# Kernel optimization log

Measured on AMD Instinct MI355X. Metric: run time of the kernel, lower is better.

The kernel has to match this reference:

```python
import jax, jax.numpy as jnp
import numpy as np

B, L, E, H = 4, 1024, 2048, 16
DH = E // H
SCALE_BASE = 512.0


def _rotate_every_two(x):
    x1 = x[..., ::2]
    x2 = x[..., 1::2]
    return jnp.stack([-x2, x1], axis=-1).reshape(x.shape)


def _xpos(x, downscale):
    # x: [BH, L, Dh]; non-incremental path => offset = 0
    length = x.shape[1]
    head_dim = x.shape[-1]
    min_pos = -(length // 2)
    positions = jnp.arange(min_pos, length + min_pos, dtype=jnp.float32)  # [L]
    base = (jnp.arange(0, head_dim, 2, dtype=jnp.float32) + 0.4 * head_dim) / (1.4 * head_dim)  # [Dh/2]
    scale = base[None, :] ** (positions[:, None] / SCALE_BASE)  # [L, Dh/2]
    # fixed_pos_embedding over `scale` (seq_len=L, dim=Dh/2), positions 0..L-1
    dim = head_dim // 2
    inv_freq = 1.0 / (10000.0 ** (jnp.arange(0, dim, dtype=jnp.float32) / dim))
    sinusoid = jnp.arange(length, dtype=jnp.float32)[:, None] * inv_freq[None, :]
    sin, cos = jnp.sin(sinusoid), jnp.cos(sinusoid)
    if downscale:
        scale = 1.0 / scale
    sin_s = jnp.repeat(sin * scale, 2, axis=-1)  # duplicate_interleave -> [L, Dh]
    cos_s = jnp.repeat(cos * scale, 2, axis=-1)
    return x * cos_s + _rotate_every_two(x) * sin_s


def setup_inputs() -> dict:
    key = jax.random.key(0)
    ks = jax.random.split(key, 6)
    w_std = 1.0 / np.sqrt(E)
    query = jax.random.normal(ks[0], (B, L, E), dtype=jnp.float32)
    Wq = jax.random.normal(ks[1], (E, E), dtype=jnp.float32) * w_std
    Wk = jax.random.normal(ks[2], (E, E), dtype=jnp.float32) * w_std
    Wv = jax.random.normal(ks[3], (E, E), dtype=jnp.float32) * w_std
    Wo = jax.random.normal(ks[4], (E, E), dtype=jnp.float32) * w_std
    bq = jnp.zeros((E,), jnp.float32)
    bk = jnp.zeros((E,), jnp.float32)
    bv = jnp.zeros((E,), jnp.float32)
    bo = jnp.zeros((E,), jnp.float32)
    # causal additive mask [L, L]: 0 on/below diag, large negative above
    attn_mask = jnp.where(jnp.triu(jnp.ones((L, L), bool), k=1), -1e9, 0.0).astype(jnp.float32)
    rel_pos = jax.random.normal(ks[5], (B * H, L, L), dtype=jnp.float32) * 0.02
    return {"query": query, "Wq": Wq, "bq": bq, "Wk": Wk, "bk": bk, "Wv": Wv,
            "bv": bv, "Wo": Wo, "bo": bo, "attn_mask": attn_mask, "rel_pos": rel_pos}


def reference(query, Wq, bq, Wk, bk, Wv, bv, Wo, bo, attn_mask, rel_pos):
    scaling = DH ** -0.5
    q = (query @ Wq.T + bq) * scaling
    k = query @ Wk.T + bk
    v = query @ Wv.T + bv

    def split(t):  # [B, L, E] -> [B*H, L, Dh]
        return t.reshape(B, L, H, DH).transpose(0, 2, 1, 3).reshape(B * H, L, DH)

    q, k, v = split(q), split(k), split(v)
    k = _xpos(k, downscale=True)
    q = _xpos(q, downscale=False)

    w = jnp.einsum('btd,bsd->bts', q, k)          # [B*H, L, L]
    w = jnp.nan_to_num(w) + attn_mask[None]
    w = w + rel_pos
    w = jax.nn.softmax(w.astype(jnp.float32), axis=-1).astype(w.dtype)
    attn = jnp.einsum('bts,bsd->btd', w, v)       # [B*H, L, Dh]
    attn = attn.reshape(B, H, L, DH).transpose(0, 2, 1, 3).reshape(B, L, E)
    out = attn @ Wo.T + bo
    attn_weights = w.reshape(B, H, L, L).transpose(1, 0, 2, 3)  # [H, B, L, L]
    return out, attn_weights
```

## Files before the change

### kernel.cpp

```cpp
#include <hip/hip_runtime.h>
#include <math.h>

#define BB 4
#define LL 1024
#define EE 2048
#define HH 16
#define DHD 128
#define NTOK 4096
#define NBH 64
#define OUT0_ELEMS 8388608

typedef __attribute__((ext_vector_type(8))) short short8;
typedef __attribute__((ext_vector_type(4))) float f32x4;
typedef __attribute__((ext_vector_type(4))) unsigned short ushort4v;
typedef __attribute__((ext_vector_type(8))) unsigned short ushort8v;

__device__ __forceinline__ unsigned short f2bf(float x) {
    union { float f; unsigned int u; } v; v.f = x;
    unsigned int r = v.u + 0x7FFFu + ((v.u >> 16) & 1u);
    return (unsigned short)(r >> 16);
}
__device__ __forceinline__ float bf2f(unsigned short h) {
    union { unsigned int u; float f; } v; v.u = ((unsigned int)h) << 16;
    return v.f;
}

__device__ __forceinline__ void gload16(const void* g, void* l) {
    __builtin_amdgcn_global_load_lds((const __attribute__((address_space(1))) void*)g,
                                     (__attribute__((address_space(3))) void*)l,
                                     16, 0, 0);
}

__global__ __launch_bounds__(256)
void cvt_all_k(const float* __restrict__ X, const float* __restrict__ Wq,
               const float* __restrict__ Wk, const float* __restrict__ Wv,
               const float* __restrict__ Wo, unsigned short* __restrict__ Xbf,
               unsigned short* __restrict__ Wqkvb, unsigned short* __restrict__ Wob) {
    size_t g = (size_t)(blockIdx.x * 256 + threadIdx.x) * 8;
    if (g >= 25165824u) return;
    const float* src;
    unsigned short* dst;
    if (g < 8388608u) {
        src = X + g; dst = Xbf + g;
    } else {
        size_t rr = g - 8388608u;
        int wi = (int)(rr >> 22);
        size_t o = rr & 4194303u;
        src = (wi == 0 ? Wq : wi == 1 ? Wk : wi == 2 ? Wv : Wo) + o;
        dst = (wi < 3 ? Wqkvb + ((size_t)wi << 22) : Wob) + o;
    }
    float4 a = *(const float4*)(src);
    float4 b = *(const float4*)(src + 4);
    ushort4v u, w;
    u.x = f2bf(a.x); u.y = f2bf(a.y); u.z = f2bf(a.z); u.w = f2bf(a.w);
    w.x = f2bf(b.x); w.y = f2bf(b.y); w.z = f2bf(b.z); w.w = f2bf(b.w);
    *(ushort4v*)(dst) = u;
    *(ushort4v*)(dst + 4) = w;
}

__global__ __launch_bounds__(64) void xpos_table_k(float4* __restrict__ tab) {
    int t = blockIdx.x;
    int j = threadIdx.x;
    float pos = (float)(t - 512);
    float base = (2.0f * (float)j + 51.2f) * (1.0f / 179.2f);
    float sc = powf(base, pos * (1.0f / 512.0f));
    float inv_freq = powf(10000.0f, -(float)j * (1.0f / 64.0f));
    float ang = (float)t * inv_freq;
    float s = sinf(ang);
    float c = cosf(ang);
    tab[(t << 6) | j] = make_float4(c * sc, s * sc, c / sc, s / sc);
}

__global__ __launch_bounds__(256)
void mmqkv_k(const unsigned short* __restrict__ Abf, const unsigned short* __restrict__ Wqkv,
             const float* __restrict__ bq, const float* __restrict__ bk,
             const float* __restrict__ bv, unsigned short* __restrict__ qb,
             unsigned short* __restrict__ kb, unsigned short* __restrict__ vt,
             const float4* __restrict__ tab, float scaling) {
    __shared__ alignas(16) unsigned short lA[128 * 32];
    __shared__ alignas(16) unsigned short lB[128 * 32];

    const int tid = threadIdx.x;
    const int lane = tid & 63;
    const int wave = tid >> 6;
    const int wr = wave >> 1, wc = wave & 1;
    const int fr = lane & 15, fq = lane >> 4;
    const int m0 = blockIdx.y * 128, n0 = blockIdx.x * 128;
    const int w = n0 >> 11;
    const float* bsel = (w == 0) ? bq : (w == 1) ? bk : bv;
    const float alpha = (w == 0) ? scaling : 1.0f;

    f32x4 acc[4][4];
#pragma unroll
    for (int i = 0; i < 4; ++i)
#pragma unroll
        for (int j = 0; j < 4; ++j) acc[i][j] = (f32x4){0.f, 0.f, 0.f, 0.f};

    for (int k0 = 0; k0 < 2048; k0 += 32) {
#pragma unroll
        for (int i = 0; i < 2; ++i) {
            int c = i * 256 + tid;
            int r = c >> 2, kc = c & 3;
            gload16(Abf + (size_t)(m0 + r) * 2048 + k0 + kc * 8, &lA[c * 8]);
        }
#pragma unroll
        for (int i = 0; i < 2; ++i) {
            int c = i * 256 + tid;
            int r = c >> 2, kc = c & 3;
            gload16(Wqkv + (size_t)(n0 + r) * 2048 + k0 + kc * 8, &lB[c * 8]);
        }
        __syncthreads();

        short8 afr[4], bfr[4];
#pragma unroll
        for (int mi = 0; mi < 4; ++mi)
            afr[mi] = *(const short8*)&lA[(wr * 64 + mi * 16 + fr) * 32 + fq * 8];
#pragma unroll
        for (int ni = 0; ni < 4; ++ni)
            bfr[ni] = *(const short8*)&lB[(wc * 64 + ni * 16 + fr) * 32 + fq * 8];
#pragma unroll
        for (int mi = 0; mi < 4; ++mi)
#pragma unroll
            for (int ni = 0; ni < 4; ++ni)
                acc[mi][ni] = __builtin_amdgcn_mfma_f32_16x16x32_bf16(
                    afr[mi], bfr[ni], acc[mi][ni], 0, 0, 0);
        __syncthreads();
    }

#pragma unroll
    for (int mi = 0; mi < 4; ++mi) {
#pragma unroll
        for (int ni = 0; ni < 4; ++ni) {
            int n = n0 + wc * 64 + ni * 16 + fr;
            int nn = n & 2047;
            int h = nn >> 7, d = nn & 127;
            float bias = bsel[nn];
#pragma unroll
            for (int r = 0; r < 4; ++r) {
                int m = m0 + wr * 64 + mi * 16 + fq * 4 + r;
                int b_ = m >> 10, t = m & 1023;
                float v = alpha * (acc[mi][ni][r] + bias);
                if (w < 2) {
                    float pv = __shfl_xor(v, 1);
                    float4 tb = tab[(t << 6) | (d >> 1)];
                    float c = (w == 0) ? tb.x : tb.z;
                    float s = (w == 0) ? tb.y : tb.w;
                    float rot = (d & 1) ? (v * c + pv * s) : (v * c - pv * s);
                    unsigned short* dst = (w == 0) ? qb : kb;
                    dst[(((size_t)(b_ * HH + h) << 10 | t) << 7) | d] = f2bf(rot);
                } else {
                    vt[((size_t)((b_ * HH + h) * 128 + d) << 10) | t] = f2bf(v);
                }
            }
        }
    }
}

__global__ __launch_bounds__(256)
void mmo_k(const unsigned short* __restrict__ Abf, const unsigned short* __restrict__ Bp,
           const float* __restrict__ bias, float* __restrict__ C) {
    __shared__ alignas(16) unsigned short lA[128 * 32];
    __shared__ alignas(16) unsigned short lB[128 * 32];

    const int tid = threadIdx.x;
    const int lane = tid & 63;
    const int wave = tid >> 6;
    const int wr = wave >> 1, wc = wave & 1;
    const int fr = lane & 15, fq = lane >> 4;
    const int m0 = blockIdx.y * 128, n0 = blockIdx.x * 128;

    f32x4 acc[4][4];
#pragma unroll
    for (int i = 0; i < 4; ++i)
#pragma unroll
        for (int j = 0; j < 4; ++j) acc[i][j] = (f32x4){0.f, 0.f, 0.f, 0.f};

    for (int k0 = 0; k0 < 2048; k0 += 32) {
#pragma unroll
        for (int i = 0; i < 2; ++i) {
            int c = i * 256 + tid;
            int r = c >> 2, kc = c & 3;
            gload16(Abf + (size_t)(m0 + r) * 2048 + k0 + kc * 8, &lA[c * 8]);
        }
#pragma unroll
        for (int i = 0; i < 2; ++i) {
            int c = i * 256 + tid;
            int r = c >> 2, kc = c & 3;
            gload16(Bp + (size_t)(n0 + r) * 2048 + k0 + kc * 8, &lB[c * 8]);
        }
        __syncthreads();

        short8 afr[4], bfr[4];
#pragma unroll
        for (int mi = 0; mi < 4; ++mi)
            afr[mi] = *(const short8*)&lA[(wr * 64 + mi * 16 + fr) * 32 + fq * 8];
#pragma unroll
        for (int ni = 0; ni < 4; ++ni)
            bfr[ni] = *(const short8*)&lB[(wc * 64 + ni * 16 + fr) * 32 + fq * 8];
#pragma unroll
        for (int mi = 0; mi < 4; ++mi)
#pragma unroll
            for (int ni = 0; ni < 4; ++ni)
                acc[mi][ni] = __builtin_amdgcn_mfma_f32_16x16x32_bf16(
                    afr[mi], bfr[ni], acc[mi][ni], 0, 0, 0);
        __syncthreads();
    }

#pragma unroll
    for (int mi = 0; mi < 4; ++mi)
#pragma unroll
        for (int ni = 0; ni < 4; ++ni)
#pragma unroll
            for (int r = 0; r < 4; ++r) {
                int m = m0 + wr * 64 + mi * 16 + fq * 4 + r;
                int n = n0 + wc * 64 + ni * 16 + fr;
                C[(size_t)m * EE + n] = acc[mi][ni][r] + bias[n];
            }
}

__global__ __launch_bounds__(256)
void scores_k(const unsigned short* __restrict__ qb, const unsigned short* __restrict__ kb,
              const float* __restrict__ rel, unsigned short* __restrict__ ebuf,
              float* __restrict__ psum) {
    __shared__ alignas(16) char smem[16384];
    unsigned short* lA = (unsigned short*)smem;
    unsigned short* lB = (unsigned short*)(smem + 8192);
    float* slab = (float*)smem;

    const int tid = threadIdx.x;
    const int lane = tid & 63, wave = tid >> 6;
    const int wr = wave >> 1, wc = wave & 1;
    const int fr = lane & 15, fq = lane >> 4;

    int idx = blockIdx.x;
    int tt = (int)((sqrtf(8.f * (float)idx + 1.f) - 1.f) * 0.5f);
    while ((tt + 1) * (tt + 2) / 2 <= idx) ++tt;
    while (tt * (tt + 1) / 2 > idx) --tt;
    const int ss = idx - tt * (tt + 1) / 2;
    const int t0 = tt << 7, s0 = ss << 7;
    const int bh = blockIdx.y;

    const unsigned short* Q = qb + ((size_t)bh << 17);
    const unsigned short* K = kb + ((size_t)bh << 17);

    f32x4 acc[4][4];
#pragma unroll
    for (int i = 0; i < 4; ++i)
#pragma unroll
        for (int j = 0; j < 4; ++j) acc[i][j] = (f32x4){0.f, 0.f, 0.f, 0.f};

    for (int k0 = 0; k0 < 128; k0 += 32) {
#pragma unroll
        for (int i = 0; i < 2; ++i) {
            int c = i * 256 + tid;
            int r = c >> 2, kc = c & 3;
            gload16(Q + (size_t)(t0 + r) * 128 + k0 + kc * 8, &lA[c * 8]);
        }
#pragma unroll
        for (int i = 0; i < 2; ++i) {
            int c = i * 256 + tid;
            int r = c >> 2, kc = c & 3;
            gload16(K + (size_t)(s0 + r) * 128 + k0 + kc * 8, &lB[c * 8]);
        }
        __syncthreads();

        short8 afr[4], bfr[4];
#pragma unroll
        for (int mi = 0; mi < 4; ++mi)
            afr[mi] = *(const short8*)&lA[(wr * 64 + mi * 16 + fr) * 32 + fq * 8];
#pragma unroll
        for (int ni = 0; ni < 4; ++ni)
            bfr[ni] = *(const short8*)&lB[(wc * 64 + ni * 16 + fr) * 32 + fq * 8];
#pragma unroll
        for (int mi = 0; mi < 4; ++mi)
#pragma unroll
            for (int ni = 0; ni < 4; ++ni)
                acc[mi][ni] = __builtin_amdgcn_mfma_f32_16x16x32_bf16(
                    afr[mi], bfr[ni], acc[mi][ni], 0, 0, 0);
        __syncthreads();
    }

    unsigned short* EO = ebuf + ((size_t)bh << 20);
    const float* RLb = rel + ((size_t)bh << 20);
#pragma unroll
    for (int sl = 0; sl < 4; ++sl) {
        if (wr == (sl >> 1)) {
#pragma unroll
            for (int mi2 = 0; mi2 < 2; ++mi2) {
                int mi = ((sl & 1) << 1) + mi2;
#pragma unroll
                for (int ni = 0; ni < 4; ++ni)
#pragma unroll
                    for (int r = 0; r < 4; ++r) {
                        int srow = (mi2 << 4) + (fq << 2) + r;
                        int col = (wc << 6) + (ni << 4) + fr;
                        slab[srow * 128 + (col ^ (((srow >> 2) & 3) << 4))] = acc[mi][ni][r];
                    }
            }
        }
        __syncthreads();
        {
            int srow = tid >> 3;
            int tg = t0 + (sl << 5) + srow;
            const float* RL = RLb + ((size_t)tg << 10) + s0;
            unsigned short* ER = EO + ((size_t)tg << 10) + s0;
            float rsum = 0.f;
#pragma unroll
            for (int c = 0; c < 4; ++c) {
                int col = ((tid & 7) << 2) + (c << 5);
                float4 sv = *(const float4*)&slab[srow * 128 + (col ^ (((srow >> 2) & 3) << 4))];
                float4 rl = *(const float4*)(RL + col);
                float4 e;
                e.x = (s0 + col     <= tg) ? __expf(sv.x + rl.x - 15.f) : 0.f;
                e.y = (s0 + col + 1 <= tg) ? __expf(sv.y + rl.y - 15.f) : 0.f;
                e.z = (s0 + col + 2 <= tg) ? __expf(sv.z + rl.z - 15.f) : 0.f;
                e.w = (s0 + col + 3 <= tg) ? __expf(sv.w + rl.w - 15.f) : 0.f;
                ushort4v h;
                h.x = f2bf(e.x); h.y = f2bf(e.y); h.z = f2bf(e.z); h.w = f2bf(e.w);
                *(ushort4v*)(ER + col) = h;
                rsum += e.x + e.y + e.z + e.w;
            }
            rsum += __shfl_xor(rsum, 1);
            rsum += __shfl_xor(rsum, 2);
            rsum += __shfl_xor(rsum, 4);
            if ((tid & 7) == 0)
                psum[((((size_t)bh << 10) + tg) << 3) + ss] = rsum;
        }
        __syncthreads();
    }
}

__global__ __launch_bounds__(256)
void pvw_k(const unsigned short* __restrict__ ebuf, const unsigned short* __restrict__ vt,
           const float* __restrict__ psum, float* __restrict__ attnP,
           unsigned short* __restrict__ am) {
    __shared__ alignas(16) unsigned short lE[64 * 64];
    __shared__ alignas(16) unsigned short lV[128 * 64];
    __shared__ float lInvF[64];

    const int tid = threadIdx.x;
    const int lane = tid & 63, wave = tid >> 6;
    const int wr = wave >> 1, wc = wave & 1;
    const int fr = lane & 15, fq = lane >> 4;
    const int strip = 15 - blockIdx.y;
    const int t0 = strip << 6;
    const int bh = blockIdx.x;
    const int hh = bh & 15, bb = bh >> 4;
    const int n_s = (t0 >> 6) + 1;

    const unsigned short* EB = ebuf + ((size_t)bh << 20) + ((size_t)t0 << 10);
    const unsigned short* Vb = vt + ((size_t)bh << 17);
    float* PO = attnP + (((size_t)(hh * BB + bb)) << 20) + ((size_t)t0 << 10);

    if (tid < 64) {
        const float* p = psum + ((((size_t)bh << 10) + t0 + tid) << 3);
        const int tt = t0 >> 7;
        float s = 0.f;
#pragma unroll
        for (int j = 0; j < 8; ++j) s += (j <= tt) ? p[j] : 0.f;
        lInvF[tid] = 1.f / s;
    }
    __syncthreads();

    f32x4 acc[2][4];
#pragma unroll
    for (int i = 0; i < 2; ++i)
#pragma unroll
        for (int j = 0; j < 4; ++j) acc[i][j] = (f32x4){0.f, 0.f, 0.f, 0.f};

    for (int j = 0; j < n_s; ++j) {
        int s0 = j << 6;
#pragma unroll
        for (int i = 0; i < 2; ++i) {
            int o = (i * 256 + tid) * 16;
            int r = o >> 7;
            int cb = (o & 127) ^ ((r & 7) << 4);
            gload16(EB + (size_t)r * 1024 + s0 + (cb >> 1), (char*)lE + o);
        }
#pragma unroll
        for (int i = 0; i < 4; ++i) {
            int o = (i * 256 + tid) * 16;
            int r = o >> 7;
            int cb = (o & 127) ^ ((r & 7) << 4);
            gload16(Vb + (size_t)r * 1024 + s0 + (cb >> 1), (char*)lV + o);
        }
        __syncthreads();

        {
            int row = tid >> 2, col0 = (tid & 3) << 4;
            float inv = lInvF[row];
            float* PR = PO + (size_t)row * 1024 + s0 + col0;
#pragma unroll
            for (int cc = 0; cc < 2; ++cc) {
                int cbyte = ((col0 + cc * 8) * 2) ^ ((row & 7) << 4);
                ushort8v ev = *(const ushort8v*)((const char*)lE + row * 128 + cbyte);
                float4 p0, p1;
                p0.x = bf2f(ev[0]) * inv; p0.y = bf2f(ev[1]) * inv;
                p0.z = bf2f(ev[2]) * inv; p0.w = bf2f(ev[3]) * inv;
                p1.x = bf2f(ev[4]) * inv; p1.y = bf2f(ev[5]) * inv;
                p1.z = bf2f(ev[6]) * inv; p1.w = bf2f(ev[7]) * inv;
                *(float4*)(PR + cc * 8) = p0;
                *(float4*)(PR + cc * 8 + 4) = p1;
            }
        }

#pragma unroll
        for (int ks = 0; ks < 2; ++ks) {
            short8 pf[2], vf[4];
#pragma unroll
            for (int mi = 0; mi < 2; ++mi) {
                int row = wr * 32 + mi * 16 + fr;
                int cb = (ks * 64 + fq * 16) ^ ((row & 7) << 4);
                pf[mi] = *(const short8*)((const char*)lE + row * 128 + cb);
            }
#pragma unroll
            for (int ni = 0; ni < 4; ++ni) {
                int row = wc * 64 + ni * 16 + fr;
                int cb = (ks * 64 + fq * 16) ^ ((row & 7) << 4);
                vf[ni] = *(const short8*)((const char*)lV + row * 128 + cb);
            }
#pragma unroll
            for (int mi = 0; mi < 2; ++mi)
#pragma unroll
                for (int ni = 0; ni < 4; ++ni)
                    acc[mi][ni] = __builtin_amdgcn_mfma_f32_16x16x32_bf16(
                        pf[mi], vf[ni], acc[mi][ni], 0, 0, 0);
        }
        __syncthreads();
    }

    {
        int row = tid >> 2;
        float4 z = make_float4(0.f, 0.f, 0.f, 0.f);
        for (int c = (n_s << 6) + ((tid & 3) << 2); c < 1024; c += 16)
            *(float4*)(PO + (size_t)row * 1024 + c) = z;
    }

#pragma unroll
    for (int mi = 0; mi < 2; ++mi)
#pragma unroll
        for (int ni = 0; ni < 4; ++ni)
#pragma unroll
            for (int r = 0; r < 4; ++r) {
                int tl = wr * 32 + mi * 16 + fq * 4 + r;
                int d = wc * 64 + ni * 16 + fr;
                float o = acc[mi][ni][r] * lInvF[tl];
                am[(((size_t)(bb * 1024 + t0 + tl)) << 11) + hh * 128 + d] = f2bf(o);
            }
}

extern "C" void kernel_launch(void* const* d_in, const int* in_sizes, int n_in,
                              void* d_out, int out_size, void* d_ws, size_t ws_size,
                              hipStream_t stream) {
    const float* query = (const float*)d_in[0];
    const float* Wq    = (const float*)d_in[1];
    const float* bq    = (const float*)d_in[2];
    const float* Wk    = (const float*)d_in[3];
    const float* bk    = (const float*)d_in[4];
    const float* Wv    = (const float*)d_in[5];
    const float* bv    = (const float*)d_in[6];
    const float* Wo    = (const float*)d_in[7];
    const float* bo    = (const float*)d_in[8];
    const float* rel   = (const float*)d_in[10];

    float* out    = (float*)d_out;
    float* attn_w = out + OUT0_ELEMS;

    char* w = (char*)d_ws;
    unsigned short* Xbf   = (unsigned short*)(w);
    unsigned short* Wqkvb = (unsigned short*)(w + (16 << 20));
    unsigned short* Wob   = (unsigned short*)(w + (40 << 20));
    unsigned short* qb    = (unsigned short*)(w + (48 << 20));
    unsigned short* kb    = (unsigned short*)(w + (64 << 20));
    unsigned short* vt    = (unsigned short*)(w + (80 << 20));
    unsigned short* am    = (unsigned short*)(w + (96 << 20));
    float4* tab           = (float4*)(w + (112 << 20));
    float* psum           = (float*)(w + (113u << 20));
    unsigned short* ebuf  = (unsigned short*)(w + (128u << 20));

    const float scaling = 0.08838834764831845f;

    xpos_table_k<<<LL, 64, 0, stream>>>(tab);

    cvt_all_k<<<12288, 256, 0, stream>>>(query, Wq, Wk, Wv, Wo, Xbf, Wqkvb, Wob);

    dim3 gqkv(3 * EE / 128, NTOK / 128);
    mmqkv_k<<<gqkv, 256, 0, stream>>>(Xbf, Wqkvb, bq, bk, bv, qb, kb, vt, tab, scaling);

    dim3 gsc(36, NBH);
    scores_k<<<gsc, 256, 0, stream>>>(qb, kb, rel, ebuf, psum);

    dim3 gpv(NBH, 16);
    pvw_k<<<gpv, 256, 0, stream>>>(ebuf, vt, psum, attn_w, am);

    dim3 gout(EE / 128, NTOK / 128);
    mmo_k<<<gout, 256, 0, stream>>>(am, Wob, bo, out);
}
```

Baseline: 472.0 us.

## Replace projection GEMMs with 256x256 double-buffered swizzled LDS pipelined kernel

Both the QKV and output projection GEMMs are replaced by a templated 8-wave kernel using 256x256 tiles, XOR-swizzled LDS, double buffering and interleaved prefetch with MFMA priority hints. The QKV epilogue stages results through LDS so xpos-rotated Q/K and transposed V are written with 16-byte vector stores instead of scattered 2-byte stores. Block indices are remapped across XCDs for better L2 locality, and the same remap is applied to the scores kernel. The large LDS footprint limits blocks per CU, and the output GEMM launches only 128 blocks.

```diff
diff --git a/kernel.cpp b/kernel.cpp
--- a/kernel.cpp
+++ b/kernel.cpp
@@ -71,151 +71,237 @@
     tab[(t << 6) | j] = make_float4(c * sc, s * sc, c / sc, s / sc);
 }
 
-__global__ __launch_bounds__(256)
-void mmqkv_k(const unsigned short* __restrict__ Abf, const unsigned short* __restrict__ Wqkv,
-             const float* __restrict__ bq, const float* __restrict__ bk,
-             const float* __restrict__ bv, unsigned short* __restrict__ qb,
-             unsigned short* __restrict__ kb, unsigned short* __restrict__ vt,
-             const float4* __restrict__ tab, float scaling) {
-    __shared__ alignas(16) unsigned short lA[128 * 32];
-    __shared__ alignas(16) unsigned short lB[128 * 32];
+template <int MODE>
+__global__ __launch_bounds__(512, 2)
+void mm8_k(const unsigned short* __restrict__ Abf, const unsigned short* __restrict__ Bw,
+           const float* __restrict__ bq, const float* __restrict__ bk,
+           const float* __restrict__ bv, unsigned short* __restrict__ qb,
+           unsigned short* __restrict__ kb, unsigned short* __restrict__ vt,
+           const float4* __restrict__ tab, float* __restrict__ Cout,
+           float scaling) {
+    __shared__ alignas(16) char smem[131072];
 
     const int tid = threadIdx.x;
     const int lane = tid & 63;
-    const int wave = tid >> 6;
-    const int wr = wave >> 1, wc = wave & 1;
+    const int wid = tid >> 6;
+    const int wr = wid >> 2;
+    const int wcn = wid & 3;
     const int fr = lane & 15, fq = lane >> 4;
-    const int m0 = blockIdx.y * 128, n0 = blockIdx.x * 128;
-    const int w = n0 >> 11;
-    const float* bsel = (w == 0) ? bq : (w == 1) ? bk : bv;
-    const float alpha = (w == 0) ? scaling : 1.0f;
-
-    f32x4 acc[4][4];
-#pragma unroll
-    for (int i = 0; i < 4; ++i)
+
+    int bx, by;
+    if constexpr (MODE == 0) {
+        const int flat = blockIdx.y * 24 + blockIdx.x;
+        const int xcd = flat & 7, rmp = flat >> 3;
+        bx = xcd * 3 + rmp % 3;
+        by = rmp / 3;
+    } else {
+        const int flat = blockIdx.y * 8 + blockIdx.x;
+        bx = flat & 7;
+        by = flat >> 3;
+    }
+    const int m0 = by * 256, n0 = bx * 256;
+
+    auto stageA = [&](int T, int half) {
+        char* dst = smem + ((T & 1) << 16) + (half << 14);
+        const unsigned short* src = Abf + (size_t)(m0 + half * 128) * 2048 + T * 64;
+#pragma unroll
+        for (int j = 0; j < 2; ++j) {
+            int o = (j * 512 + tid) * 16;
+            int r = o >> 7;
+            int cs = ((o & 127) >> 4) ^ (r & 7);
+            gload16(src + (size_t)r * 2048 + cs * 8, dst + o);
+        }
+    };
+    auto stageB = [&](int T, int half) {
+        char* dst = smem + ((T & 1) << 16) + 32768 + (half << 14);
+        const unsigned short* src = Bw + (size_t)(n0 + half * 128) * 2048 + T * 64;
+#pragma unroll
+        for (int j = 0; j < 2; ++j) {
+            int o = (j * 512 + tid) * 16;
+            int r = o >> 7;
+            int cs = ((o & 127) >> 4) ^ (r & 7);
+            gload16(src + (size_t)r * 2048 + cs * 8, dst + o);
+        }
+    };
+    auto rdA = [&](int buf, int mi, int ks) -> short8 {
+        int rl = mi * 16 + fr;
+        const char* base = smem + (buf << 16) + (wr << 14);
+        return *(const short8*)(base + rl * 128 + ((ks * 4 + fq) ^ (rl & 7)) * 16);
+    };
+    auto rdB = [&](int buf, int ni, int ks) -> short8 {
+        int rb = ((wcn & 1) << 6) + ni * 16 + fr;
+        const char* base = smem + (buf << 16) + 32768 + ((wcn >> 1) << 14);
+        return *(const short8*)(base + rb * 128 + ((ks * 4 + fq) ^ (rb & 7)) * 16);
+    };
+
+    f32x4 acc[8][4];
+#pragma unroll
+    for (int i = 0; i < 8; ++i)
 #pragma unroll
         for (int j = 0; j < 4; ++j) acc[i][j] = (f32x4){0.f, 0.f, 0.f, 0.f};
 
-    for (int k0 = 0; k0 < 2048; k0 += 32) {
-#pragma unroll
-        for (int i = 0; i < 2; ++i) {
-            int c = i * 256 + tid;
-            int r = c >> 2, kc = c & 3;
-            gload16(Abf + (size_t)(m0 + r) * 2048 + k0 + kc * 8, &lA[c * 8]);
-        }
-#pragma unroll
-        for (int i = 0; i < 2; ++i) {
-            int c = i * 256 + tid;
-            int r = c >> 2, kc = c & 3;
-            gload16(Wqkv + (size_t)(n0 + r) * 2048 + k0 + kc * 8, &lB[c * 8]);
-        }
-        __syncthreads();
-
-        short8 afr[4], bfr[4];
+    stageA(0, 0); stageA(0, 1); stageB(0, 0); stageB(0, 1);
+    stageB(1, 0); stageB(1, 1);
+
+    for (int T = 0; T < 32; ++T) {
+        const int buf = T & 1;
+        if (T < 31) asm volatile("s_waitcnt vmcnt(4)" ::: "memory");
+        else        asm volatile("s_waitcnt vmcnt(0)" ::: "memory");
+        __builtin_amdgcn_s_barrier();
+
+        short8 af[2][4], bf[2][4];
+
+#pragma unroll
+        for (int mi = 0; mi < 4; ++mi) { af[0][mi] = rdA(buf, mi, 0); af[1][mi] = rdA(buf, mi, 1); }
+#pragma unroll
+        for (int ni = 0; ni < 2; ++ni) { bf[0][ni] = rdB(buf, ni, 0); bf[1][ni] = rdB(buf, ni, 1); }
+        if (T < 31) stageA(T + 1, 0);
+        __builtin_amdgcn_s_barrier();
+        __builtin_amdgcn_s_setprio(1);
 #pragma unroll
         for (int mi = 0; mi < 4; ++mi)
-            afr[mi] = *(const short8*)&lA[(wr * 64 + mi * 16 + fr) * 32 + fq * 8];
-#pragma unroll
-        for (int ni = 0; ni < 4; ++ni)
-            bfr[ni] = *(const short8*)&lB[(wc * 64 + ni * 16 + fr) * 32 + fq * 8];
+#pragma unroll
+            for (int ni = 0; ni < 2; ++ni) {
+                acc[mi][ni] = __builtin_amdgcn_mfma_f32_16x16x32_bf16(af[0][mi], bf[0][ni], acc[mi][ni], 0, 0, 0);
+                acc[mi][ni] = __builtin_amdgcn_mfma_f32_16x16x32_bf16(af[1][mi], bf[1][ni], acc[mi][ni], 0, 0, 0);
+            }
+        __builtin_amdgcn_s_setprio(0);
+        __builtin_amdgcn_s_barrier();
+
+#pragma unroll
+        for (int ni = 2; ni < 4; ++ni) { bf[0][ni] = rdB(buf, ni, 0); bf[1][ni] = rdB(buf, ni, 1); }
+        if (T < 31) stageA(T + 1, 1);
+        __builtin_amdgcn_s_barrier();
+        __builtin_amdgcn_s_setprio(1);
 #pragma unroll
         for (int mi = 0; mi < 4; ++mi)
 #pragma unroll
+            for (int ni = 2; ni < 4; ++ni) {
+                acc[mi][ni] = __builtin_amdgcn_mfma_f32_16x16x32_bf16(af[0][mi], bf[0][ni], acc[mi][ni], 0, 0, 0);
+                acc[mi][ni] = __builtin_amdgcn_mfma_f32_16x16x32_bf16(af[1][mi], bf[1][ni], acc[mi][ni], 0, 0, 0);
+            }
+        __builtin_amdgcn_s_setprio(0);
+        __builtin_amdgcn_s_barrier();
+
+#pragma unroll
+        for (int mi = 0; mi < 4; ++mi) { af[0][mi] = rdA(buf, mi + 4, 0); af[1][mi] = rdA(buf, mi + 4, 1); }
+        if (T < 30) stageB(T + 2, 0);
+        __builtin_amdgcn_s_barrier();
+        __builtin_amdgcn_s_setprio(1);
+#pragma unroll
+        for (int mi = 0; mi < 4; ++mi)
+#pragma unroll
+            for (int ni = 2; ni < 4; ++ni) {
+                acc[mi + 4][ni] = __builtin_amdgcn_mfma_f32_16x16x32_bf16(af[0][mi], bf[0][ni], acc[mi + 4][ni], 0, 0, 0);
+                acc[mi + 4][ni] = __builtin_amdgcn_mfma_f32_16x16x32_bf16(af[1][mi], bf[1][ni], acc[mi + 4][ni], 0, 0, 0);
+            }
+        __builtin_amdgcn_s_setprio(0);
+        __builtin_amdgcn_s_barrier();
+
+        if (T < 30) stageB(T + 2, 1);
+        __builtin_amdgcn_s_barrier();
+        __builtin_amdgcn_s_setprio(1);
+#pragma unroll
+        for (int mi = 0; mi < 4; ++mi)
+#pragma unroll
+            for (int ni = 0; ni < 2; ++ni) {
+                acc[mi + 4][ni] = __builtin_amdgcn_mfma_f32_16x16x32_bf16(af[0][mi], bf[0][ni], acc[mi + 4][ni], 0, 0, 0);
+                acc[mi + 4][ni] = __builtin_amdgcn_mfma_f32_16x16x32_bf16(af[1][mi], bf[1][ni], acc[mi + 4][ni], 0, 0, 0);
+            }
+        __builtin_amdgcn_s_setprio(0);
+        __builtin_amdgcn_s_barrier();
+    }
+
+    if constexpr (MODE == 1) {
+        const float* bias = bq;
+#pragma unroll
+        for (int mi = 0; mi < 8; ++mi)
+#pragma unroll
             for (int ni = 0; ni < 4; ++ni)
-                acc[mi][ni] = __builtin_amdgcn_mfma_f32_16x16x32_bf16(
-                    afr[mi], bfr[ni], acc[mi][ni], 0, 0, 0);
-        __syncthreads();
-    }
-
-#pragma unroll
-    for (int mi = 0; mi < 4; ++mi) {
-#pragma unroll
-        for (int ni = 0; ni < 4; ++ni) {
-            int n = n0 + wc * 64 + ni * 16 + fr;
-            int nn = n & 2047;
-            int h = nn >> 7, d = nn & 127;
-            float bias = bsel[nn];
-#pragma unroll
-            for (int r = 0; r < 4; ++r) {
-                int m = m0 + wr * 64 + mi * 16 + fq * 4 + r;
-                int b_ = m >> 10, t = m & 1023;
-                float v = alpha * (acc[mi][ni][r] + bias);
-                if (w < 2) {
-                    float pv = __shfl_xor(v, 1);
-                    float4 tb = tab[(t << 6) | (d >> 1)];
+#pragma unroll
+                for (int rg = 0; rg < 4; ++rg) {
+                    int m = m0 + wr * 128 + mi * 16 + fq * 4 + rg;
+                    int n = n0 + wcn * 64 + ni * 16 + fr;
+                    Cout[(size_t)m * EE + n] = acc[mi][ni][rg] + bias[n];
+                }
+        return;
+    } else {
+        const int w = n0 >> 11;
+        const float* bsel = (w == 0) ? bq : (w == 1) ? bk : bv;
+        const float alpha = (w == 0) ? scaling : 1.0f;
+        const int hbase = (n0 & 2047) >> 7;
+        const int b_ = m0 >> 10;
+        const int m0r = m0 & 1023;
+        float* slab = (float*)smem;
+
+        unsigned short* qk = (w == 0) ? qb : kb;
+#pragma unroll
+        for (int sl = 0; sl < 8; ++sl) {
+            if (wr == (sl >> 2)) {
+#pragma unroll
+                for (int mi2 = 0; mi2 < 2; ++mi2) {
+                    int mi = ((sl & 3) << 1) + mi2;
+#pragma unroll
+                    for (int ni = 0; ni < 4; ++ni) {
+                        int scol = wcn * 64 + ni * 16 + fr;
+                        float bias = bsel[(n0 & 2047) + scol];
+#pragma unroll
+                        for (int rg = 0; rg < 4; ++rg) {
+                            int srow = (mi2 << 4) + fq * 4 + rg;
+                            slab[srow * 260 + scol] = alpha * (acc[mi][ni][rg] + bias);
+                        }
+                    }
+                }
+            }
+            __syncthreads();
+
+            if (w < 2) {
+                int sr = tid >> 4, cg = tid & 15;
+                int t = m0r + (sl << 5) + sr;
+                int h = hbase + (cg >> 3);
+                int d0 = (cg & 7) << 4;
+                const float* SR = slab + sr * 260 + cg * 16;
+                ushort8v h0, h1;
+#pragma unroll
+                for (int p = 0; p < 4; ++p) {
+                    float x = SR[2 * p], y = SR[2 * p + 1];
+                    float4 tb = tab[(t << 6) | ((d0 >> 1) + p)];
                     float c = (w == 0) ? tb.x : tb.z;
                     float s = (w == 0) ? tb.y : tb.w;
-                    float rot = (d & 1) ? (v * c + pv * s) : (v * c - pv * s);
-                    unsigned short* dst = (w == 0) ? qb : kb;
-                    dst[(((size_t)(b_ * HH + h) << 10 | t) << 7) | d] = f2bf(rot);
-                } else {
-                    vt[((size_t)((b_ * HH + h) * 128 + d) << 10) | t] = f2bf(v);
+                    h0[2 * p]     = f2bf(x * c - y * s);
+                    h0[2 * p + 1] = f2bf(y * c + x * s);
                 }
-            }
-        }
-    }
-}
-
-__global__ __launch_bounds__(256)
-void mmo_k(const unsigned short* __restrict__ Abf, const unsigned short* __restrict__ Bp,
-           const float* __restrict__ bias, float* __restrict__ C) {
-    __shared__ alignas(16) unsigned short lA[128 * 32];
-    __shared__ alignas(16) unsigned short lB[128 * 32];
-
-    const int tid = threadIdx.x;
-    const int lane = tid & 63;
-    const int wave = tid >> 6;
-    const int wr = wave >> 1, wc = wave & 1;
-    const int fr = lane & 15, fq = lane >> 4;
-    const int m0 = blockIdx.y * 128, n0 = blockIdx.x * 128;
-
-    f32x4 acc[4][4];
-#pragma unroll
-    for (int i = 0; i < 4; ++i)
-#pragma unroll
-        for (int j = 0; j < 4; ++j) acc[i][j] = (f32x4){0.f, 0.f, 0.f, 0.f};
-
-    for (int k0 = 0; k0 < 2048; k0 += 32) {
-#pragma unroll
-        for (int i = 0; i < 2; ++i) {
-            int c = i * 256 + tid;
-            int r = c >> 2, kc = c & 3;
-            gload16(Abf + (size_t)(m0 + r) * 2048 + k0 + kc * 8, &lA[c * 8]);
-        }
-#pragma unroll
-        for (int i = 0; i < 2; ++i) {
-            int c = i * 256 + tid;
-            int r = c >> 2, kc = c & 3;
-            gload16(Bp + (size_t)(n0 + r) * 2048 + k0 + kc * 8, &lB[c * 8]);
-        }
-        __syncthreads();
-
-        short8 afr[4], bfr[4];
-#pragma unroll
-        for (int mi = 0; mi < 4; ++mi)
-            afr[mi] = *(const short8*)&lA[(wr * 64 + mi * 16 + fr) * 32 + fq * 8];
-#pragma unroll
-        for (int ni = 0; ni < 4; ++ni)
-            bfr[ni] = *(const short8*)&lB[(wc * 64 + ni * 16 + fr) * 32 + fq * 8];
-#pragma unroll
-        for (int mi = 0; mi < 4; ++mi)
-#pragma unroll
-            for (int ni = 0; ni < 4; ++ni)
-                acc[mi][ni] = __builtin_amdgcn_mfma_f32_16x16x32_bf16(
-                    afr[mi], bfr[ni], acc[mi][ni], 0, 0, 0);
-        __syncthreads();
-    }
-
-#pragma unroll
-    for (int mi = 0; mi < 4; ++mi)
-#pragma unroll
-        for (int ni = 0; ni < 4; ++ni)
-#pragma unroll
-            for (int r = 0; r < 4; ++r) {
-                int m = m0 + wr * 64 + mi * 16 + fq * 4 + r;
-                int n = n0 + wc * 64 + ni * 16 + fr;
-                C[(size_t)m * EE + n] = acc[mi][ni][r] + bias[n];
-            }
+#pragma unroll
+                for (int p = 0; p < 4; ++p) {
+                    float x = SR[8 + 2 * p], y = SR[8 + 2 * p + 1];
+                    float4 tb = tab[(t << 6) | ((d0 >> 1) + 4 + p)];
+                    float c = (w == 0) ? tb.x : tb.z;
+                    float s = (w == 0) ? tb.y : tb.w;
+                    h1[2 * p]     = f2bf(x * c - y * s);
+                    h1[2 * p + 1] = f2bf(y * c + x * s);
+                }
+                unsigned short* DR = qk + (((size_t)(b_ * HH + h)) << 17) + ((size_t)t << 7) + d0;
+                *(ushort8v*)(DR) = h0;
+                *(ushort8v*)(DR + 8) = h1;
+            } else {
+                int vcol = tid >> 1, th = tid & 1;
+                int h = hbase + (vcol >> 7), d = vcol & 127;
+                ushort8v h0, h1;
+#pragma unroll
+                for (int p = 0; p < 8; ++p)
+                    h0[p] = f2bf(slab[(th * 16 + p) * 260 + vcol]);
+#pragma unroll
+                for (int p = 0; p < 8; ++p)
+                    h1[p] = f2bf(slab[(th * 16 + 8 + p) * 260 + vcol]);
+                unsigned short* DR = vt + (((size_t)((b_ * HH + h) * 128 + d)) << 10)
+                                     + m0r + (sl << 5);
+                DR += th * 16;
+                *(ushort8v*)(DR) = h0;
+                *(ushort8v*)(DR + 8) = h1;
+            }
+            __syncthreads();
+        }
+    }
 }
 
 __global__ __launch_bounds__(256)
@@ -232,13 +318,16 @@
     const int wr = wave >> 1, wc = wave & 1;
     const int fr = lane & 15, fq = lane >> 4;
 
-    int idx = blockIdx.x;
+    const int flat = blockIdx.y * 36 + blockIdx.x;
+    const int xcd = flat & 7, rmp = flat >> 3;
+    int idx = rmp % 36;
+    const int bh = (rmp / 36) * 8 + xcd;
+
     int tt = (int)((sqrtf(8.f * (float)idx + 1.f) - 1.f) * 0.5f);
     while ((tt + 1) * (tt + 2) / 2 <= idx) ++tt;
     while (tt * (tt + 1) / 2 > idx) --tt;
     const int ss = idx - tt * (tt + 1) / 2;
     const int t0 = tt << 7, s0 = ss << 7;
-    const int bh = blockIdx.y;
 
     const unsigned short* Q = qb + ((size_t)bh << 17);
     const unsigned short* K = kb + ((size_t)bh << 17);
@@ -484,8 +573,9 @@
 
     cvt_all_k<<<12288, 256, 0, stream>>>(query, Wq, Wk, Wv, Wo, Xbf, Wqkvb, Wob);
 
-    dim3 gqkv(3 * EE / 128, NTOK / 128);
-    mmqkv_k<<<gqkv, 256, 0, stream>>>(Xbf, Wqkvb, bq, bk, bv, qb, kb, vt, tab, scaling);
+    dim3 gqkv(24, 16);
+    mm8_k<0><<<gqkv, 512, 0, stream>>>(Xbf, Wqkvb, bq, bk, bv, qb, kb, vt, tab,
+                                       nullptr, scaling);
 
     dim3 gsc(36, NBH);
     scores_k<<<gsc, 256, 0, stream>>>(qb, kb, rel, ebuf, psum);
@@ -493,6 +583,7 @@
     dim3 gpv(NBH, 16);
     pvw_k<<<gpv, 256, 0, stream>>>(ebuf, vt, psum, attn_w, am);
 
-    dim3 gout(EE / 128, NTOK / 128);
-    mmo_k<<<gout, 256, 0, stream>>>(am, Wob, bo, out);
-}
+    dim3 gout(8, 16);
+    mm8_k<1><<<gout, 512, 0, stream>>>(am, Wob, bo, nullptr, nullptr, nullptr,
+                                       nullptr, nullptr, tab, out, 1.0f);
+}
```

New measurement: 456.6 us. -3.3%, faster.
